# Performance work log

Hardware: AMD Instinct MI355X
Metric: run time of the kernel (lower is better)

Reference implementation:

```python
import jax, jax.numpy as jnp
import numpy as np

B, T, DIM, H = 4, 2048, 512, 8
DECAY = 0.9

def setup_inputs():
    key = jax.random.key(0)
    ks = jax.random.split(key, 8)
    s = 1.0 / np.sqrt(DIM)
    def lin(k):
        return jax.random.normal(k, (DIM, DIM), jnp.float32) * s
    return {
        "q": jax.random.normal(ks[0], (B, T, DIM), jnp.float32),
        "k": jax.random.normal(ks[1], (B, T, DIM), jnp.float32),
        "v": jax.random.normal(ks[2], (B, T, DIM), jnp.float32),
        "Wa": lin(ks[3]), "ba": jnp.zeros((DIM,), jnp.float32),
        "Wb": lin(ks[4]), "bb": jnp.zeros((DIM,), jnp.float32),
        "Wg": lin(ks[5]), "bg": jnp.zeros((DIM,), jnp.float32),
        "Wo": lin(ks[6]), "bo": jnp.zeros((DIM,), jnp.float32),
    }

def _linear_scan(a, b):
    # h_t = a_t * h_{t-1} + b_t along time axis=1, via associative scan
    def combine(c1, c2):
        a1, b1 = c1
        a2, b2 = c2
        return a1 * a2, a2 * b1 + b2
    return jax.lax.associative_scan(combine, (a, b), axis=1)[1]

def reference(q, k, v, Wa, ba, Wb, bb, Wg, bg, Wo, bo):
    # --- Mamba-style selective scan on q (no residual) ---
    a = jax.nn.sigmoid(q @ Wa + ba)   # input-dependent decay [B,T,D]
    b = q @ Wb + bb                   # input injection       [B,T,D]
    h = _linear_scan(a, b)            # recurrent state       [B,T,D]
    g = jax.nn.sigmoid(q @ Wg + bg)   # gate
    m_out = (h * g) @ Wo + bo         # [B,T,D]

    # --- RetNet-style decay-weighted linear retention ---
    Dh = DIM // H
    qh = q.reshape(B, T, H, Dh)
    kh = k.reshape(B, T, H, Dh)
    vh = v.reshape(B, T, H, Dh)
    t = jnp.arange(T)
    delta = t[:, None] - t[None, :]           # t - s
    mask = delta >= 0                         # causal
    decay_mat = jnp.where(
        mask,
        jnp.exp(jnp.where(mask, delta, 0).astype(jnp.float32) * np.float32(np.log(DECAY))),
        0.0,
    )                                          # [T,T]
    scores = jnp.einsum('bthd,bshd->bhts', qh, kh) * decay_mat  # [B,H,T,T]
    r_out = jnp.einsum('bhts,bshd->bthd', scores, vh).reshape(B, T, DIM)

    return m_out + r_out
```

## Files before the change

kernel.cpp:

```cpp
#include <hip/hip_runtime.h>
#include <hip/hip_bf16.h>

typedef unsigned short u16;

#define BB 4
#define TT 2048
#define DIM 512
#define NH 8
#define DH 64
#define DECAY 0.9f

#define CC 64
#define NC 32
#define BHN 32

#define CHS 32
#define NSC 64

#define TM 128
#define TN 128
#define BK 64

#define SS 72

typedef __attribute__((ext_vector_type(8))) short bf16x8;
typedef __attribute__((ext_vector_type(4))) float f32x4;

__device__ __forceinline__ u16 f2bfu(float f) {
  union { float f; unsigned int u; } c; c.f = f;
  unsigned int u = c.u + 0x7FFFu + ((c.u >> 16) & 1u);
  return (u16)(u >> 16);
}
__device__ __forceinline__ float bf2f(u16 u) {
  union { unsigned int u; float f; } c; c.u = ((unsigned int)u) << 16;
  return c.f;
}

__device__ __forceinline__ void gl_lds16(const void* g, void* l) {
  __builtin_amdgcn_global_load_lds(
      (const __attribute__((address_space(1))) void*)g,
      (__attribute__((address_space(3))) void*)(unsigned int)(unsigned long long)l,
      16, 0, 0);
}

__device__ __forceinline__ void gemm_tile(
    int nTile, int mTile, const u16* __restrict__ A, const u16* __restrict__ Bt,
    const float* __restrict__ b0, const float* __restrict__ b1,
    const float* __restrict__ b2,
    u16* __restrict__ C0, u16* __restrict__ C1, u16* __restrict__ C2,
    int act_mask, u16* As, u16* Bs, int tid) {
  int wave = tid >> 6, lane = tid & 63;
  int group = (nTile * TN) >> 9;
  const float* bias = (group == 0) ? b0 : (group == 1) ? b1 : b2;
  u16* C = (group == 0) ? C0 : (group == 1) ? C1 : C2;
  int act = (act_mask >> group) & 1;

  int wm = (wave >> 1) * 64, wn = (wave & 1) * 64;
  int rowA = lane & 15, khalf = lane >> 4;

  f32x4 acc[4][4];
#pragma unroll
  for (int i = 0; i < 4; ++i)
#pragma unroll
    for (int j = 0; j < 4; ++j) acc[i][j] = (f32x4){0.f, 0.f, 0.f, 0.f};

  const u16* Abase = A + (size_t)mTile * TM * 512;
  const u16* Bbase = Bt + (size_t)nTile * TN * 512;

  for (int kk = 0; kk < 512; kk += BK) {
#pragma unroll
    for (int i = 0; i < 4; ++i) {
      int o = (wave * 4 + i) * 64 + lane;
      int row = o >> 3, gk = (o & 7) ^ (row & 7);
      gl_lds16(Abase + (size_t)row * 512 + kk + gk * 8, &As[o * 8]);
    }
#pragma unroll
    for (int i = 0; i < 4; ++i) {
      int o = (wave * 4 + i) * 64 + lane;
      int row = o >> 3, gk = (o & 7) ^ (row & 7);
      gl_lds16(Bbase + (size_t)row * 512 + kk + gk * 8, &Bs[o * 8]);
    }
    __syncthreads();
#pragma unroll
    for (int k0 = 0; k0 < 2; ++k0) {
      bf16x8 af[4], bfr[4];
#pragma unroll
      for (int mi = 0; mi < 4; ++mi) {
        int rr = wm + mi * 16 + rowA;
        int gk = k0 * 4 + khalf;
        int o = rr * 8 + (gk ^ (rr & 7));
        af[mi] = *(const bf16x8*)&As[o * 8];
      }
#pragma unroll
      for (int ni = 0; ni < 4; ++ni) {
        int rr = wn + ni * 16 + rowA;
        int gk = k0 * 4 + khalf;
        int o = rr * 8 + (gk ^ (rr & 7));
        bfr[ni] = *(const bf16x8*)&Bs[o * 8];
      }
#pragma unroll
      for (int mi = 0; mi < 4; ++mi)
#pragma unroll
        for (int ni = 0; ni < 4; ++ni)
          acc[mi][ni] = __builtin_amdgcn_mfma_f32_16x16x32_bf16(
              af[mi], bfr[ni], acc[mi][ni], 0, 0, 0);
    }
    __syncthreads();
  }
  int cloc = lane & 15, rq = (lane >> 4) * 4;
#pragma unroll
  for (int mi = 0; mi < 4; ++mi) {
#pragma unroll
    for (int r = 0; r < 4; ++r) {
      int m = mTile * TM + wm + mi * 16 + rq + r;
#pragma unroll
      for (int ni = 0; ni < 4; ++ni) {
        int n = (nTile * TN + wn + ni * 16 + cloc) & 511;
        float vv = acc[mi][ni][r] + bias[n];
        if (act) vv = 1.0f / (1.0f + __expf(-vv));
        C[(size_t)m * 512 + n] = f2bfu(vv);
      }
    }
  }
}

__device__ __forceinline__ void gemm_tile64(
    int nTile, int mTile, const u16* __restrict__ A, const u16* __restrict__ Bt,
    const float* __restrict__ bias, float* __restrict__ C,
    const u16* __restrict__ Radd, u16* As, u16* Bs, int tid) {
  int wave = tid >> 6, lane = tid & 63;
  int wm = wave * 32;
  int rowA = lane & 15, khalf = lane >> 4;

  f32x4 acc[2][4];
#pragma unroll
  for (int i = 0; i < 2; ++i)
#pragma unroll
    for (int j = 0; j < 4; ++j) acc[i][j] = (f32x4){0.f, 0.f, 0.f, 0.f};

  const u16* Abase = A + (size_t)mTile * TM * 512;
  const u16* Bbase = Bt + (size_t)nTile * 64 * 512;

  for (int kk = 0; kk < 512; kk += BK) {
#pragma unroll
    for (int i = 0; i < 4; ++i) {
      int o = (wave * 4 + i) * 64 + lane;
      int row = o >> 3, gk = (o & 7) ^ (row & 7);
      gl_lds16(Abase + (size_t)row * 512 + kk + gk * 8, &As[o * 8]);
    }
#pragma unroll
    for (int i = 0; i < 2; ++i) {
      int o = (wave * 2 + i) * 64 + lane;
      int row = o >> 3, gk = (o & 7) ^ (row & 7);
      gl_lds16(Bbase + (size_t)row * 512 + kk + gk * 8, &Bs[o * 8]);
    }
    __syncthreads();
#pragma unroll
    for (int k0 = 0; k0 < 2; ++k0) {
      bf16x8 af[2], bfr[4];
#pragma unroll
      for (int mi = 0; mi < 2; ++mi) {
        int rr = wm + mi * 16 + rowA;
        int gk = k0 * 4 + khalf;
        int o = rr * 8 + (gk ^ (rr & 7));
        af[mi] = *(const bf16x8*)&As[o * 8];
      }
#pragma unroll
      for (int ni = 0; ni < 4; ++ni) {
        int rr = ni * 16 + rowA;
        int gk = k0 * 4 + khalf;
        int o = rr * 8 + (gk ^ (rr & 7));
        bfr[ni] = *(const bf16x8*)&Bs[o * 8];
      }
#pragma unroll
      for (int mi = 0; mi < 2; ++mi)
#pragma unroll
        for (int ni = 0; ni < 4; ++ni)
          acc[mi][ni] = __builtin_amdgcn_mfma_f32_16x16x32_bf16(
              af[mi], bfr[ni], acc[mi][ni], 0, 0, 0);
    }
    __syncthreads();
  }
  int cloc = lane & 15, rq = (lane >> 4) * 4;
#pragma unroll
  for (int mi = 0; mi < 2; ++mi) {
#pragma unroll
    for (int r = 0; r < 4; ++r) {
      int m = mTile * TM + wm + mi * 16 + rq + r;
#pragma unroll
      for (int ni = 0; ni < 4; ++ni) {
        int n = nTile * 64 + ni * 16 + cloc;
        float vv = acc[mi][ni][r] + bias[n] + bf2f(Radd[(size_t)m * 512 + n]);
        C[(size_t)m * 512 + n] = vv;
      }
    }
  }
}

__device__ __forceinline__ void dev_retscan(int unit, int tid,
    const u16* __restrict__ KVTb, u16* __restrict__ Ptb) {
  int gid = unit * 256 + tid;
  int bh = gid >> 12, ed = gid & 4095;
  float carry = 0.f;
  const float dC = __powf(DECAY, (float)CC);
#pragma unroll
  for (int c = 0; c < NC; ++c) {
    size_t idx = ((size_t)(c * BHN + bh)) * 4096 + ed;
    Ptb[idx] = f2bfu(carry);
    carry = fmaf(dC, carry, bf2f(KVTb[idx]));
  }
}

__device__ __forceinline__ void dev_part(int unit, int tid,
    const u16* __restrict__ Ab16, const u16* __restrict__ Bb16,
    float* __restrict__ SA, float* __restrict__ SB) {
  int ci = unit >> 3, grp = unit & 7;
  int ch = grp * 256 + tid;
  int bb2 = ch >> 9, d = ch & 511;
  size_t base = ((size_t)bb2 * TT + ci * CHS) * DIM + d;
  float h = 0.f, pA = 1.f;
#pragma unroll
  for (int t = 0; t < CHS; ++t) {
    float av = bf2f(Ab16[base + (size_t)t * DIM]);
    float bv = bf2f(Bb16[base + (size_t)t * DIM]);
    h = fmaf(av, h, bv);
    pA *= av;
  }
  SA[ci * 2048 + ch] = pA;
  SB[ci * 2048 + ch] = h;
}

__device__ __forceinline__ void dev_apply(int unit, int tid,
    const u16* __restrict__ Ab16, const u16* __restrict__ Bb16,
    const u16* __restrict__ g, const float* __restrict__ SA,
    const float* __restrict__ SB, u16* __restrict__ hg) {
  int ci = unit >> 3, grp = unit & 7;
  int ch = grp * 256 + tid;
  int bb = ch >> 9, d = ch & 511;
  float carry = 0.f;
  for (int p = 0; p < ci; ++p)
    carry = fmaf(SA[p * 2048 + ch], carry, SB[p * 2048 + ch]);
  size_t base = ((size_t)bb * TT + ci * CHS) * DIM + d;
  float h = carry;
#pragma unroll
  for (int t = 0; t < CHS; ++t) {
    size_t idx = base + (size_t)t * DIM;
    h = fmaf(bf2f(Ab16[idx]), h, bf2f(Bb16[idx]));
    hg[idx] = f2bfu(h * bf2f(g[idx]));
  }
}

__device__ __forceinline__ void dev_retout(int unit, int tid,
    u16* Sa, float* dp, float* dpi,
    const u16* __restrict__ qbf, const u16* __restrict__ kcb,
    const u16* __restrict__ VTg, const u16* __restrict__ Ptb,
    u16* __restrict__ routb) {
  int bh = unit & 31, c = unit >> 5;
  int b = bh >> 3, h = bh & 7;
  int wave = tid >> 6, lane = tid & 63;
  size_t base = ((size_t)(b * TT + c * CC)) * DIM + h * DH;
  if (tid < 66) dp[tid] = __powf(DECAY, (float)tid);
  if (tid < 64) dpi[tid] = __powf(DECAY, (float)tid - 63.0f);

  int wm = (wave >> 1) * 32, wn = (wave & 1) * 32;
  int rowA = lane & 15, khalf = lane >> 4;

  bf16x8 afq[2][2];
#pragma unroll
  for (int k0 = 0; k0 < 2; ++k0)
#pragma unroll
    for (int mi = 0; mi < 2; ++mi)
      afq[k0][mi] = *(const bf16x8*)(qbf + base +
          (size_t)(wm + mi * 16 + rowA) * 512 + (k0 * 4 + khalf) * 8);
  const u16* kcbase = kcb + ((size_t)bh * NC + c) * 64 * 64;
  bf16x8 bfk[2][2];
#pragma unroll
  for (int k0 = 0; k0 < 2; ++k0)
#pragma unroll
    for (int ni = 0; ni < 2; ++ni)
      bfk[k0][ni] = *(const bf16x8*)(kcbase +
          (size_t)(wn + ni * 16 + rowA) * 64 + (k0 * 4 + khalf) * 8);

  f32x4 accS[2][2];
#pragma unroll
  for (int i = 0; i < 2; ++i)
#pragma unroll
    for (int j = 0; j < 2; ++j) accS[i][j] = (f32x4){0.f, 0.f, 0.f, 0.f};
#pragma unroll
  for (int k0 = 0; k0 < 2; ++k0)
#pragma unroll
    for (int mi = 0; mi < 2; ++mi)
#pragma unroll
      for (int ni = 0; ni < 2; ++ni)
        accS[mi][ni] = __builtin_amdgcn_mfma_f32_16x16x32_bf16(
            afq[k0][mi], bfk[k0][ni], accS[mi][ni], 0, 0, 0);
  __syncthreads();

  int cloc = lane & 15, rq = (lane >> 4) * 4;
#pragma unroll
  for (int mi = 0; mi < 2; ++mi)
#pragma unroll
    for (int ni = 0; ni < 2; ++ni)
#pragma unroll
      for (int r = 0; r < 4; ++r) {
        int i = wm + mi * 16 + rq + r;
        int j = wn + ni * 16 + cloc;
        float sv = (j <= i) ? accS[mi][ni][r] * dpi[i] : 0.f;
        Sa[i * SS + j] = f2bfu(sv);
      }
#pragma unroll
  for (int mi = 0; mi < 2; ++mi) {
    float s = dp[wm + mi * 16 + rowA + 1];
#pragma unroll
    for (int k0 = 0; k0 < 2; ++k0) {
      bf16x8 t = afq[k0][mi];
#pragma unroll
      for (int u = 0; u < 8; ++u)
        t[u] = (short)f2bfu(bf2f((u16)t[u]) * s);
      afq[k0][mi] = t;
    }
  }
  __syncthreads();

  f32x4 accO[2][2];
#pragma unroll
  for (int i = 0; i < 2; ++i)
#pragma unroll
    for (int j = 0; j < 2; ++j) accO[i][j] = (f32x4){0.f, 0.f, 0.f, 0.f};
#pragma unroll
  for (int k0 = 0; k0 < 4; ++k0) {
    bf16x8 af[2], bfv[2];
#pragma unroll
    for (int mi = 0; mi < 2; ++mi) {
      if (k0 < 2)
        af[mi] = *(const bf16x8*)&Sa[(wm + mi * 16 + rowA) * SS +
                                     (k0 * 4 + khalf) * 8];
      else
        af[mi] = afq[k0 - 2][mi];
    }
#pragma unroll
    for (int ni = 0; ni < 2; ++ni) {
      int e = wn + ni * 16 + rowA;
      if (k0 < 2)
        bfv[ni] = *(const bf16x8*)(VTg + ((size_t)bh * 64 + e) * TT + c * 64 +
                                   (k0 * 4 + khalf) * 8);
      else
        bfv[ni] = *(const bf16x8*)(Ptb + ((size_t)(c * BHN + bh)) * 4096 +
                                   e * 64 + ((k0 - 2) * 4 + khalf) * 8);
    }
#pragma unroll
    for (int mi = 0; mi < 2; ++mi)
#pragma unroll
      for (int ni = 0; ni < 2; ++ni)
        accO[mi][ni] = __builtin_amdgcn_mfma_f32_16x16x32_bf16(
            af[mi], bfv[ni], accO[mi][ni], 0, 0, 0);
  }
#pragma unroll
  for (int mi = 0; mi < 2; ++mi)
#pragma unroll
    for (int r = 0; r < 4; ++r) {
      int i = wm + mi * 16 + rq + r;
#pragma unroll
      for (int ni = 0; ni < 2; ++ni) {
        int e = wn + ni * 16 + cloc;
        routb[base + (size_t)i * 512 + e] = f2bfu(accO[mi][ni][r]);
      }
    }
}

__global__ __launch_bounds__(256) void k1_prep_retkv(
    const float* __restrict__ q, u16* __restrict__ qbf,
    const float* __restrict__ W0, const float* __restrict__ W1,
    const float* __restrict__ W2, const float* __restrict__ W3,
    u16* __restrict__ Wt,
    const float* __restrict__ k, const float* __restrict__ v,
    u16* __restrict__ KVTb, u16* __restrict__ VTg, u16* __restrict__ kcb) {
  __shared__ __align__(16) u16 smem[2 * 64 * SS];
  __shared__ float t[32][33];
  int bx = blockIdx.x, tid = threadIdx.x;
  if (bx < 1024) {
    int bh = bx & 31, c = bx >> 5;
    int b = bh >> 3, h = bh & 7;
    int wave = tid >> 6, lane = tid & 63;
    u16* VT = smem;
    u16* KT = smem + 64 * SS;
    size_t base = ((size_t)(b * TT + c * CC)) * DIM + h * DH;
    int row = tid >> 2, part = tid & 3, e0 = part * 16;
    float w = __powf(DECAY, (float)(63 - row));
    __align__(16) u16 krow[16];
    {
      const float4* vs = (const float4*)(v + base + (size_t)row * DIM + e0);
      const float4* ks = (const float4*)(k + base + (size_t)row * DIM + e0);
#pragma unroll
      for (int u4 = 0; u4 < 4; ++u4) {
        float4 fv = vs[u4], fk = ks[u4];
        VT[(e0 + u4 * 4 + 0) * SS + row] = f2bfu(fv.x);
        VT[(e0 + u4 * 4 + 1) * SS + row] = f2bfu(fv.y);
        VT[(e0 + u4 * 4 + 2) * SS + row] = f2bfu(fv.z);
        VT[(e0 + u4 * 4 + 3) * SS + row] = f2bfu(fv.w);
        u16 k0s = f2bfu(fk.x * w), k1s = f2bfu(fk.y * w);
        u16 k2s = f2bfu(fk.z * w), k3s = f2bfu(fk.w * w);
        KT[(e0 + u4 * 4 + 0) * SS + row] = k0s;
        KT[(e0 + u4 * 4 + 1) * SS + row] = k1s;
        KT[(e0 + u4 * 4 + 2) * SS + row] = k2s;
        KT[(e0 + u4 * 4 + 3) * SS + row] = k3s;
        krow[u4 * 4 + 0] = k0s; krow[u4 * 4 + 1] = k1s;
        krow[u4 * 4 + 2] = k2s; krow[u4 * 4 + 3] = k3s;
      }
    }
    {
      u16* kdst = kcb + (((size_t)bh * NC + c) * 64 + row) * 64 + e0;
      *(uint4*)kdst = *(const uint4*)&krow[0];
      *(uint4*)(kdst + 8) = *(const uint4*)&krow[8];
    }
    __syncthreads();
    {
      int e = row;
      u16* dst = VTg + ((size_t)bh * 64 + e) * TT + c * 64 + part * 16;
      *(uint4*)dst = *(const uint4*)&VT[e * SS + part * 16];
      *(uint4*)(dst + 8) = *(const uint4*)&VT[e * SS + part * 16 + 8];
    }
    int wm = (wave >> 1) * 32, wn = (wave & 1) * 32;
    int rowA = lane & 15, khalf = lane >> 4;
    f32x4 acc[2][2];
#pragma unroll
    for (int i = 0; i < 2; ++i)
#pragma unroll
      for (int j = 0; j < 2; ++j) acc[i][j] = (f32x4){0.f, 0.f, 0.f, 0.f};
#pragma unroll
    for (int k0 = 0; k0 < 2; ++k0) {
      int gk = k0 * 4 + khalf;
      bf16x8 af[2], bfr[2];
#pragma unroll
      for (int mi = 0; mi < 2; ++mi)
        af[mi] = *(const bf16x8*)&VT[(wm + mi * 16 + rowA) * SS + gk * 8];
#pragma unroll
      for (int ni = 0; ni < 2; ++ni)
        bfr[ni] = *(const bf16x8*)&KT[(wn + ni * 16 + rowA) * SS + gk * 8];
#pragma unroll
      for (int mi = 0; mi < 2; ++mi)
#pragma unroll
        for (int ni = 0; ni < 2; ++ni)
          acc[mi][ni] = __builtin_amdgcn_mfma_f32_16x16x32_bf16(
              af[mi], bfr[ni], acc[mi][ni], 0, 0, 0);
    }
    int cloc = lane & 15, rq = (lane >> 4) * 4;
    u16* o = KVTb + ((size_t)(c * BHN + bh)) * 4096;
#pragma unroll
    for (int mi = 0; mi < 2; ++mi)
#pragma unroll
      for (int r = 0; r < 4; ++r) {
        int e = wm + mi * 16 + rq + r;
#pragma unroll
        for (int ni = 0; ni < 2; ++ni)
          o[e * 64 + (wn + ni * 16 + cloc)] = f2bfu(acc[mi][ni][r]);
      }
  } else if (bx < 2048) {
    int bx2 = bx - 1024;
    int m = bx2 >> 8, rem = bx2 & 255;
    int n0 = (rem & 15) * 32, k0 = (rem >> 4) * 32;
    const float* W = (m == 0) ? W0 : (m == 1) ? W1 : (m == 2) ? W2 : W3;
    int tx = tid & 31, ty = tid >> 5;
#pragma unroll
    for (int r = 0; r < 32; r += 8)
      t[ty + r][tx] = W[(size_t)(k0 + ty + r) * DIM + n0 + tx];
    __syncthreads();
    u16* o = Wt + (size_t)m * DIM * DIM;
#pragma unroll
    for (int r = 0; r < 32; r += 8)
      o[(size_t)(n0 + ty + r) * DIM + k0 + tx] = f2bfu(t[tx][ty + r]);
  } else {
    int i0 = ((bx - 2048) * 256 + tid) * 2;
#pragma unroll
    for (int u2 = 0; u2 < 2; ++u2) {
      float4 f = ((const float4*)q)[i0 + u2];
      ushort4 u;
      u.x = f2bfu(f.x); u.y = f2bfu(f.y); u.z = f2bfu(f.z); u.w = f2bfu(f.w);
      ((ushort4*)qbf)[i0 + u2] = u;
    }
  }
}

__global__ __launch_bounds__(256) void k2_gemm1_retscan(
    const u16* __restrict__ qbf, const u16* __restrict__ WtAll,
    const float* __restrict__ ba, const float* __restrict__ bb,
    const float* __restrict__ bg,
    u16* __restrict__ Ab16, u16* __restrict__ Bb16, u16* __restrict__ Gb16,
    const u16* __restrict__ KVTb, u16* __restrict__ Ptb) {
  __shared__ __align__(16) u16 smem[TM * BK + TN * BK];
  int bx = blockIdx.x, tid = threadIdx.x;
  if (bx < 768) {
    int r = bx & 7, t6 = bx >> 3;
    int nT = t6 % 12, s = t6 / 12;
    int mT = (s << 3) | r;
    gemm_tile(nT, mT, qbf, WtAll, ba, bb, bg, Ab16, Bb16, Gb16,
              0b101, smem, smem + TM * BK, tid);
  } else {
    dev_retscan(bx - 768, tid, KVTb, Ptb);
  }
}

__global__ __launch_bounds__(256) void k3_part_retout(
    const u16* __restrict__ Ab16, const u16* __restrict__ Bb16,
    float* __restrict__ SA, float* __restrict__ SB,
    const u16* __restrict__ qbf, const u16* __restrict__ kcb,
    const u16* __restrict__ VTg, const u16* __restrict__ Ptb,
    u16* __restrict__ routb) {
  __shared__ __align__(16) u16 Sa[64 * SS];
  __shared__ float dp[66];
  __shared__ float dpi[64];
  int bx = blockIdx.x, tid = threadIdx.x;
  if (bx < 512) {
    dev_part(bx, tid, Ab16, Bb16, SA, SB);
    return;
  }
  dev_retout(bx - 512, tid, Sa, dp, dpi, qbf, kcb, VTg, Ptb, routb);
}

__global__ __launch_bounds__(256) void k4_apply_retout(
    const u16* __restrict__ Ab16, const u16* __restrict__ Bb16,
    const u16* __restrict__ g, const float* __restrict__ SA,
    const float* __restrict__ SB, u16* __restrict__ hg,
    const u16* __restrict__ qbf, const u16* __restrict__ kcb,
    const u16* __restrict__ VTg, const u16* __restrict__ Ptb,
    u16* __restrict__ routb) {
  __shared__ __align__(16) u16 Sa[64 * SS];
  __shared__ float dp[66];
  __shared__ float dpi[64];
  int bx = blockIdx.x, tid = threadIdx.x;
  if (bx < 512) {
    dev_apply(bx, tid, Ab16, Bb16, g, SA, SB, hg);
    return;
  }
  dev_retout(bx, tid, Sa, dp, dpi, qbf, kcb, VTg, Ptb, routb);
}

__global__ __launch_bounds__(256) void k5_gemm2(
    const u16* __restrict__ hgbf, const u16* __restrict__ Wto,
    const float* __restrict__ bo, float* __restrict__ out,
    const u16* __restrict__ routb) {
  __shared__ __align__(16) u16 smem[TM * BK + 64 * BK];
  int bx = blockIdx.x;
  int r = bx & 7, t6 = bx >> 3;
  int nT = t6 & 7, s = t6 >> 3;
  int mT = (s << 3) | r;
  gemm_tile64(nT, mT, hgbf, Wto, bo, out, routb,
              smem, smem + TM * BK, threadIdx.x);
}

extern "C" void kernel_launch(void* const* d_in, const int* in_sizes, int n_in,
                              void* d_out, int out_size, void* d_ws, size_t ws_size,
                              hipStream_t stream) {
  const float* q  = (const float*)d_in[0];
  const float* k  = (const float*)d_in[1];
  const float* v  = (const float*)d_in[2];
  const float* Wa = (const float*)d_in[3];
  const float* ba = (const float*)d_in[4];
  const float* Wb = (const float*)d_in[5];
  const float* bb = (const float*)d_in[6];
  const float* Wg = (const float*)d_in[7];
  const float* bg = (const float*)d_in[8];
  const float* Wo = (const float*)d_in[9];
  const float* bo = (const float*)d_in[10];
  float* out = (float*)d_out;
  float* ws = (float*)d_ws;

  const size_t NEL = (size_t)BB * TT * DIM;
  float* SA = ws;
  float* SB = SA + (size_t)NSC * 2048;
  u16* up = (u16*)(SB + (size_t)NSC * 2048);
  u16* Ab16  = up;  up += NEL;
  u16* Bb16  = up;  up += NEL;
  u16* Gb16  = up;  up += NEL;
  u16* qbf   = up;  up += NEL;
  u16* hgbf  = up;  up += NEL;
  u16* WtAll = up;  up += 4 * DIM * DIM;
  u16* KVTb  = up;  up += (size_t)NC * BHN * 4096;
  u16* Ptb   = up;  up += (size_t)NC * BHN * 4096;
  u16* VTg   = up;  up += (size_t)BHN * 64 * TT;
  u16* routb = up;  up += NEL;
  u16* kcb   = up;  up += (size_t)BHN * NC * 64 * 64;

  k1_prep_retkv<<<4096, 256, 0, stream>>>(q, qbf, Wa, Wb, Wg, Wo, WtAll,
                                          k, v, KVTb, VTg, kcb);

  k2_gemm1_retscan<<<1280, 256, 0, stream>>>(qbf, WtAll, ba, bb, bg,
                                             Ab16, Bb16, Gb16, KVTb, Ptb);

  k3_part_retout<<<1024, 256, 0, stream>>>(Ab16, Bb16, SA, SB,
                                           qbf, kcb, VTg, Ptb, routb);

  k4_apply_retout<<<1024, 256, 0, stream>>>(Ab16, Bb16, Gb16, SA, SB, hgbf,
                                            qbf, kcb, VTg, Ptb, routb);

  k5_gemm2<<<512, 256, 0, stream>>>(hgbf, WtAll + 3 * DIM * DIM,
                                    bo, out, routb);
}
```

Before: 176.5 us.

## Vectorize scan passes to two channels per thread and halve scan chunk length

The retention-state scan, chunk-partial scan and apply pass now each process two adjacent channels per thread using 32-bit loads and stores. The chunk length drops from 32 to 16 steps with twice as many chunks, and the per-chunk (product, state) pairs are packed into one float4 array. The q-to-bf16 conversion handles four float4s per thread, which reduces the prep grid, and retention blocks are placed before scan blocks in the fused kernels. The aim is fewer, wider memory transactions and less serial latency per thread, at the cost of a longer sequential carry loop in the apply pass.

```diff
diff --git a/kernel.cpp b/kernel.cpp
--- a/kernel.cpp
+++ b/kernel.cpp
@@ -14,8 +14,8 @@
 #define NC 32
 #define BHN 32
 
-#define CHS 32
-#define NSC 64
+#define CHS 16
+#define NSC 128
 
 #define TM 128
 #define TN 128
@@ -197,56 +197,72 @@
   }
 }
 
-__device__ __forceinline__ void dev_retscan(int unit, int tid,
+
+__device__ __forceinline__ void dev_retscan2(int unit, int tid,
     const u16* __restrict__ KVTb, u16* __restrict__ Ptb) {
   int gid = unit * 256 + tid;
-  int bh = gid >> 12, ed = gid & 4095;
-  float carry = 0.f;
+  int bh = gid >> 11, edp = gid & 2047;
+  int ed0 = edp * 2;
+  float c0 = 0.f, c1 = 0.f;
   const float dC = __powf(DECAY, (float)CC);
 #pragma unroll
   for (int c = 0; c < NC; ++c) {
-    size_t idx = ((size_t)(c * BHN + bh)) * 4096 + ed;
-    Ptb[idx] = f2bfu(carry);
-    carry = fmaf(dC, carry, bf2f(KVTb[idx]));
-  }
-}
-
-__device__ __forceinline__ void dev_part(int unit, int tid,
+    size_t idx = ((size_t)(c * BHN + bh)) * 4096 + ed0;
+    unsigned int kv = *(const unsigned int*)&KVTb[idx];
+    unsigned int o = (unsigned int)f2bfu(c0) | ((unsigned int)f2bfu(c1) << 16);
+    *(unsigned int*)&Ptb[idx] = o;
+    c0 = fmaf(dC, c0, bf2f((u16)kv));
+    c1 = fmaf(dC, c1, bf2f((u16)(kv >> 16)));
+  }
+}
+
+__device__ __forceinline__ void dev_part2(int unit, int tid,
     const u16* __restrict__ Ab16, const u16* __restrict__ Bb16,
-    float* __restrict__ SA, float* __restrict__ SB) {
-  int ci = unit >> 3, grp = unit & 7;
-  int ch = grp * 256 + tid;
-  int bb2 = ch >> 9, d = ch & 511;
+    float4* __restrict__ SAB) {
+  int ci = unit >> 2, grp = unit & 3;
+  int cp = grp * 256 + tid;
+  int ch0 = cp * 2;
+  int bb2 = ch0 >> 9, d = ch0 & 511;
   size_t base = ((size_t)bb2 * TT + ci * CHS) * DIM + d;
-  float h = 0.f, pA = 1.f;
+  float h0 = 0.f, h1 = 0.f, p0 = 1.f, p1 = 1.f;
 #pragma unroll
   for (int t = 0; t < CHS; ++t) {
-    float av = bf2f(Ab16[base + (size_t)t * DIM]);
-    float bv = bf2f(Bb16[base + (size_t)t * DIM]);
-    h = fmaf(av, h, bv);
-    pA *= av;
-  }
-  SA[ci * 2048 + ch] = pA;
-  SB[ci * 2048 + ch] = h;
-}
-
-__device__ __forceinline__ void dev_apply(int unit, int tid,
+    unsigned int av = *(const unsigned int*)&Ab16[base + (size_t)t * DIM];
+    unsigned int bv = *(const unsigned int*)&Bb16[base + (size_t)t * DIM];
+    float a0 = bf2f((u16)av), a1 = bf2f((u16)(av >> 16));
+    h0 = fmaf(a0, h0, bf2f((u16)bv));
+    h1 = fmaf(a1, h1, bf2f((u16)(bv >> 16)));
+    p0 *= a0; p1 *= a1;
+  }
+  SAB[(size_t)ci * 1024 + cp] = make_float4(p0, h0, p1, h1);
+}
+
+__device__ __forceinline__ void dev_apply2(int unit, int tid,
     const u16* __restrict__ Ab16, const u16* __restrict__ Bb16,
-    const u16* __restrict__ g, const float* __restrict__ SA,
-    const float* __restrict__ SB, u16* __restrict__ hg) {
-  int ci = unit >> 3, grp = unit & 7;
-  int ch = grp * 256 + tid;
-  int bb = ch >> 9, d = ch & 511;
-  float carry = 0.f;
-  for (int p = 0; p < ci; ++p)
-    carry = fmaf(SA[p * 2048 + ch], carry, SB[p * 2048 + ch]);
+    const u16* __restrict__ g, const float4* __restrict__ SAB,
+    u16* __restrict__ hg) {
+  int ci = unit >> 2, grp = unit & 3;
+  int cp = grp * 256 + tid;
+  int ch0 = cp * 2;
+  int bb = ch0 >> 9, d = ch0 & 511;
+  float c0 = 0.f, c1 = 0.f;
+  for (int p = 0; p < ci; ++p) {
+    float4 s = SAB[(size_t)p * 1024 + cp];
+    c0 = fmaf(s.x, c0, s.y);
+    c1 = fmaf(s.z, c1, s.w);
+  }
   size_t base = ((size_t)bb * TT + ci * CHS) * DIM + d;
-  float h = carry;
 #pragma unroll
   for (int t = 0; t < CHS; ++t) {
     size_t idx = base + (size_t)t * DIM;
-    h = fmaf(bf2f(Ab16[idx]), h, bf2f(Bb16[idx]));
-    hg[idx] = f2bfu(h * bf2f(g[idx]));
+    unsigned int av = *(const unsigned int*)&Ab16[idx];
+    unsigned int bv = *(const unsigned int*)&Bb16[idx];
+    unsigned int gv = *(const unsigned int*)&g[idx];
+    c0 = fmaf(bf2f((u16)av), c0, bf2f((u16)bv));
+    c1 = fmaf(bf2f((u16)(av >> 16)), c1, bf2f((u16)(bv >> 16)));
+    unsigned int o = (unsigned int)f2bfu(c0 * bf2f((u16)gv)) |
+                     ((unsigned int)f2bfu(c1 * bf2f((u16)(gv >> 16))) << 16);
+    *(unsigned int*)&hg[idx] = o;
   }
 }
 
@@ -470,9 +486,9 @@
     for (int r = 0; r < 32; r += 8)
       o[(size_t)(n0 + ty + r) * DIM + k0 + tx] = f2bfu(t[tx][ty + r]);
   } else {
-    int i0 = ((bx - 2048) * 256 + tid) * 2;
-#pragma unroll
-    for (int u2 = 0; u2 < 2; ++u2) {
+    int i0 = ((bx - 2048) * 256 + tid) * 4;
+#pragma unroll
+    for (int u2 = 0; u2 < 4; ++u2) {
       float4 f = ((const float4*)q)[i0 + u2];
       ushort4 u;
       u.x = f2bfu(f.x); u.y = f2bfu(f.y); u.z = f2bfu(f.z); u.w = f2bfu(f.w);
@@ -496,13 +512,13 @@
     gemm_tile(nT, mT, qbf, WtAll, ba, bb, bg, Ab16, Bb16, Gb16,
               0b101, smem, smem + TM * BK, tid);
   } else {
-    dev_retscan(bx - 768, tid, KVTb, Ptb);
-  }
-}
-
-__global__ __launch_bounds__(256) void k3_part_retout(
+    dev_retscan2(bx - 768, tid, KVTb, Ptb);
+  }
+}
+
+__global__ __launch_bounds__(256) void k3_retout_part(
     const u16* __restrict__ Ab16, const u16* __restrict__ Bb16,
-    float* __restrict__ SA, float* __restrict__ SB,
+    float4* __restrict__ SAB,
     const u16* __restrict__ qbf, const u16* __restrict__ kcb,
     const u16* __restrict__ VTg, const u16* __restrict__ Ptb,
     u16* __restrict__ routb) {
@@ -510,17 +526,17 @@
   __shared__ float dp[66];
   __shared__ float dpi[64];
   int bx = blockIdx.x, tid = threadIdx.x;
-  if (bx < 512) {
-    dev_part(bx, tid, Ab16, Bb16, SA, SB);
+  if (bx >= 512) {
+    dev_part2(bx - 512, tid, Ab16, Bb16, SAB);
     return;
   }
-  dev_retout(bx - 512, tid, Sa, dp, dpi, qbf, kcb, VTg, Ptb, routb);
-}
-
-__global__ __launch_bounds__(256) void k4_apply_retout(
+  dev_retout(bx, tid, Sa, dp, dpi, qbf, kcb, VTg, Ptb, routb);
+}
+
+__global__ __launch_bounds__(256) void k4_retout_apply(
     const u16* __restrict__ Ab16, const u16* __restrict__ Bb16,
-    const u16* __restrict__ g, const float* __restrict__ SA,
-    const float* __restrict__ SB, u16* __restrict__ hg,
+    const u16* __restrict__ g, const float4* __restrict__ SAB,
+    u16* __restrict__ hg,
     const u16* __restrict__ qbf, const u16* __restrict__ kcb,
     const u16* __restrict__ VTg, const u16* __restrict__ Ptb,
     u16* __restrict__ routb) {
@@ -528,11 +544,11 @@
   __shared__ float dp[66];
   __shared__ float dpi[64];
   int bx = blockIdx.x, tid = threadIdx.x;
-  if (bx < 512) {
-    dev_apply(bx, tid, Ab16, Bb16, g, SA, SB, hg);
+  if (bx >= 512) {
+    dev_apply2(bx - 512, tid, Ab16, Bb16, g, SAB, hg);
     return;
   }
-  dev_retout(bx, tid, Sa, dp, dpi, qbf, kcb, VTg, Ptb, routb);
+  dev_retout(bx + 512, tid, Sa, dp, dpi, qbf, kcb, VTg, Ptb, routb);
 }
 
 __global__ __launch_bounds__(256) void k5_gemm2(
@@ -563,12 +579,10 @@
   const float* Wo = (const float*)d_in[9];
   const float* bo = (const float*)d_in[10];
   float* out = (float*)d_out;
-  float* ws = (float*)d_ws;
 
   const size_t NEL = (size_t)BB * TT * DIM;
-  float* SA = ws;
-  float* SB = SA + (size_t)NSC * 2048;
-  u16* up = (u16*)(SB + (size_t)NSC * 2048);
+  float4* SAB = (float4*)d_ws;
+  u16* up = (u16*)(SAB + (size_t)NSC * 1024);
   u16* Ab16  = up;  up += NEL;
   u16* Bb16  = up;  up += NEL;
   u16* Gb16  = up;  up += NEL;
@@ -581,16 +595,16 @@
   u16* routb = up;  up += NEL;
   u16* kcb   = up;  up += (size_t)BHN * NC * 64 * 64;
 
-  k1_prep_retkv<<<4096, 256, 0, stream>>>(q, qbf, Wa, Wb, Wg, Wo, WtAll,
+  k1_prep_retkv<<<3072, 256, 0, stream>>>(q, qbf, Wa, Wb, Wg, Wo, WtAll,
                                           k, v, KVTb, VTg, kcb);
 
-  k2_gemm1_retscan<<<1280, 256, 0, stream>>>(qbf, WtAll, ba, bb, bg,
+  k2_gemm1_retscan<<<1024, 256, 0, stream>>>(qbf, WtAll, ba, bb, bg,
                                              Ab16, Bb16, Gb16, KVTb, Ptb);
 
-  k3_part_retout<<<1024, 256, 0, stream>>>(Ab16, Bb16, SA, SB,
+  k3_retout_part<<<1024, 256, 0, stream>>>(Ab16, Bb16, SAB,
                                            qbf, kcb, VTg, Ptb, routb);
 
-  k4_apply_retout<<<1024, 256, 0, stream>>>(Ab16, Bb16, Gb16, SA, SB, hgbf,
+  k4_retout_apply<<<1024, 256, 0, stream>>>(Ab16, Bb16, Gb16, SAB, hgbf,
                                             qbf, kcb, VTg, Ptb, routb);
 
   k5_gemm2<<<512, 256, 0, stream>>>(hgbf, WtAll + 3 * DIM * DIM,
```

Result: slower. 197.4 us (+11.9%).
